# Performance work log

Hardware: AMD Instinct MI355X
Metric: run time of the kernel (lower is better)

## Reference

```python
import jax, jax.numpy as jnp
import numpy as np

B, N, S, VOCAB, D, NNZ = 16, 2048, 4096, 50257, 128, 1048576


def setup_inputs() -> dict:
    key = jax.random.key(0)
    k1, k2, k3, k4, k5, k6 = jax.random.split(key, 6)
    return {
        "subnode_ids": jax.random.randint(k1, (B, S), 0, VOCAB),
        "mask_batch": jax.random.randint(k2, (NNZ,), 0, B),
        "mask_node": jax.random.randint(k3, (NNZ,), 0, N),
        "mask_subnode": jax.random.randint(k4, (NNZ,), 0, S),
        "mask_values": jax.random.uniform(k5, (NNZ,), dtype=jnp.float32),
        "emb_table": jax.random.normal(k6, (VOCAB, D), dtype=jnp.float32),
    }


def reference(subnode_ids, mask_batch, mask_node, mask_subnode, mask_values, emb_table):
    # Gather token embeddings for every (batch, subnode) slot: [B, S, D] -> [B*S, D]
    subnode_emb = emb_table[subnode_ids].reshape(B * S, D)
    # Flattened COO indices (same as batch*max_nodes + node, batch*max_subnodes + subnode)
    row = mask_batch * N + mask_node      # destination node slot in [0, B*N)
    col = mask_batch * S + mask_subnode   # source subnode slot in [0, B*S)
    # Fused gather + weighted scatter-add (== sparse.mm of expanded_mask @ subnode_emb)
    contrib = subnode_emb[col] * mask_values[:, None]           # [NNZ, D]
    pooled = jax.ops.segment_sum(contrib, row, num_segments=B * N)  # [B*N, D]
    return pooled.reshape(B, N, D)
```

## Files before the change

### kernel.cpp

```cpp
#include <hip/hip_runtime.h>
#include <hip/hip_fp16.h>

#define Bq 16
#define Nq 2048
#define Sq 4096
#define Dq 128
#define VOCABq 50257
#define NNZq 1048576
#define ROWS (Bq * Nq)
#define NBIN 2048
#define RPB 16
#define BCAP 768
#define OVF_MAX 65536
#define BTPB 1024
#define BEPT 4

typedef unsigned long long u64;
typedef float vfloat4 __attribute__((ext_vector_type(4)));
typedef unsigned short vushort4 __attribute__((ext_vector_type(4)));
typedef unsigned short vushort8 __attribute__((ext_vector_type(8)));

__global__ __launch_bounds__(256) void cast_kernel(
    const float* __restrict__ emb, unsigned short* __restrict__ emb16)
{
    const int NQUAD = (VOCABq * Dq) / 4;
    int i = blockIdx.x * 256 + threadIdx.x;
    if (i >= NQUAD) return;
    vfloat4 f = reinterpret_cast<const vfloat4*>(emb)[i];
    vushort4 h;
    h.x = __half_as_ushort(__float2half_rn(f.x));
    h.y = __half_as_ushort(__float2half_rn(f.y));
    h.z = __half_as_ushort(__float2half_rn(f.z));
    h.w = __half_as_ushort(__float2half_rn(f.w));
    __builtin_nontemporal_store(h, reinterpret_cast<vushort4*>(emb16) + i);
}

__global__ __launch_bounds__(BTPB) void bin_kernel(
    const int* __restrict__ subnode_ids,
    const int* __restrict__ mb,
    const int* __restrict__ mn,
    const int* __restrict__ ms,
    const float* __restrict__ mv,
    int* __restrict__ binCnt,
    u64* __restrict__ binMem,
    int* __restrict__ ovfn,
    int* __restrict__ ovf)
{
    __shared__ int hist[NBIN];
    __shared__ int base[NBIN];
    int t = threadIdx.x;
    for (int g = t; g < NBIN; g += BTPB) hist[g] = 0;
    __syncthreads();

    int blockBase = blockIdx.x * (BTPB * BEPT);
    int g[BEPT], rank[BEPT];
    u64 pk[BEPT];
    #pragma unroll
    for (int k = 0; k < BEPT; k++) {
        int i   = blockBase + k * BTPB + t;
        int b   = mb[i];
        int row = b * Nq + mn[i];
        int tok = subnode_ids[b * Sq + ms[i]];
        float v = mv[i];
        g[k]  = row >> 4;
        pk[k] = ((u64)(unsigned)__float_as_int(v) << 32)
              | ((u64)(row & 15) << 16)
              | (unsigned)tok;
        rank[k] = atomicAdd(&hist[g[k]], 1);
    }
    __syncthreads();
    for (int gg = t; gg < NBIN; gg += BTPB) {
        int h = hist[gg];
        base[gg] = h ? atomicAdd(&binCnt[gg], h) : 0;
    }
    __syncthreads();
    #pragma unroll
    for (int k = 0; k < BEPT; k++) {
        int p = base[g[k]] + rank[k];
        if (p < BCAP) {
            binMem[(size_t)g[k] * BCAP + p] = pk[k];
        } else {
            int o = atomicAdd(ovfn, 1);
            if (o < OVF_MAX) ovf[o] = blockBase + k * BTPB + t;
        }
    }
}

__global__ __launch_bounds__(256) void pool_kernel(
    const unsigned short* __restrict__ emb16,
    const int* __restrict__ binCnt,
    const u64* __restrict__ binMem,
    float* __restrict__ out)
{
    __shared__ u64 ebuf[BCAP];
    __shared__ int hist[64];
    __shared__ int start[65];
    __shared__ int cursor[64];

    int t   = threadIdx.x;
    int bin = blockIdx.x;
    if (t < 64) hist[t] = 0;
    __syncthreads();

    int n = min(binCnt[bin], BCAP);
    const u64* bm = binMem + (size_t)bin * BCAP;

    u64 myPk[3];
    int myKey[3], myCnt = 0;
    for (int e = t; e < n; e += 256) {
        u64 pk  = bm[e];
        int tok = (int)(pk & 0xFFFF);
        int key = ((tok >> 14) << 4) | (int)((pk >> 16) & 15);
        myPk[myCnt] = pk; myKey[myCnt] = key; myCnt++;
        atomicAdd(&hist[key], 1);
    }
    __syncthreads();
    if (t < 64) {
        int v = hist[t];
        #pragma unroll
        for (int d = 1; d < 64; d <<= 1) {
            int w = __shfl_up(v, d, 64);
            if (t >= d) v += w;
        }
        start[t + 1] = v;
        if (t == 0) start[0] = 0;
    }
    __syncthreads();
    if (t < 64) cursor[t] = start[t];
    __syncthreads();
    for (int k = 0; k < myCnt; k++) {
        int p = atomicAdd(&cursor[myKey[k]], 1);
        ebuf[p] = myPk[k];
    }
    __syncthreads();

    int g    = t >> 4;
    int lane = t & 15;
    vfloat4 a0 = {0.f, 0.f, 0.f, 0.f};
    vfloat4 a1 = {0.f, 0.f, 0.f, 0.f};
    #pragma unroll
    for (int q = 0; q < 4; q++) {
        int s0 = start[q * 16 + g], s1 = start[q * 16 + g + 1];
        int k = s0;
        for (; k + 8 <= s1; k += 8) {
            int   tk[8];
            float vv[8];
            #pragma unroll
            for (int u = 0; u < 8; u++) {
                u64 pk = ebuf[k + u];
                tk[u] = (int)(pk & 0xFFFF);
                vv[u] = __int_as_float((int)(pk >> 32));
            }
            vushort8 e[8];
            #pragma unroll
            for (int u = 0; u < 8; u++)
                e[u] = reinterpret_cast<const vushort8*>(emb16 + (size_t)tk[u] * Dq)[lane];
            #pragma unroll
            for (int u = 0; u < 8; u++) {
                a0.x += __half2float(__ushort_as_half(e[u][0])) * vv[u];
                a0.y += __half2float(__ushort_as_half(e[u][1])) * vv[u];
                a0.z += __half2float(__ushort_as_half(e[u][2])) * vv[u];
                a0.w += __half2float(__ushort_as_half(e[u][3])) * vv[u];
                a1.x += __half2float(__ushort_as_half(e[u][4])) * vv[u];
                a1.y += __half2float(__ushort_as_half(e[u][5])) * vv[u];
                a1.z += __half2float(__ushort_as_half(e[u][6])) * vv[u];
                a1.w += __half2float(__ushort_as_half(e[u][7])) * vv[u];
            }
        }
        for (; k < s1; k++) {
            u64 pk = ebuf[k];
            int   tok = (int)(pk & 0xFFFF);
            float v   = __int_as_float((int)(pk >> 32));
            vushort8 e = reinterpret_cast<const vushort8*>(emb16 + (size_t)tok * Dq)[lane];
            a0.x += __half2float(__ushort_as_half(e[0])) * v;
            a0.y += __half2float(__ushort_as_half(e[1])) * v;
            a0.z += __half2float(__ushort_as_half(e[2])) * v;
            a0.w += __half2float(__ushort_as_half(e[3])) * v;
            a1.x += __half2float(__ushort_as_half(e[4])) * v;
            a1.y += __half2float(__ushort_as_half(e[5])) * v;
            a1.z += __half2float(__ushort_as_half(e[6])) * v;
            a1.w += __half2float(__ushort_as_half(e[7])) * v;
        }
    }
    float* orow = out + ((size_t)bin * RPB + g) * Dq + lane * 8;
    __builtin_nontemporal_store(a0, reinterpret_cast<vfloat4*>(orow));
    __builtin_nontemporal_store(a1, reinterpret_cast<vfloat4*>(orow) + 1);
}

__global__ __launch_bounds__(256) void overflow_kernel(
    const int* __restrict__ subnode_ids,
    const int* __restrict__ mb, const int* __restrict__ mn,
    const int* __restrict__ ms, const float* __restrict__ mv,
    const float* __restrict__ emb,
    const int* __restrict__ ovfn, const int* __restrict__ ovf,
    float* __restrict__ out)
{
    int nov = min(*ovfn, OVF_MAX);
    for (int e = blockIdx.x * 256 + threadIdx.x; e < nov; e += gridDim.x * 256) {
        int i = ovf[e];
        int b = mb[i];
        int row = b * Nq + mn[i];
        int tok = subnode_ids[b * Sq + ms[i]];
        float v = mv[i];
        const float* src = emb + (size_t)tok * Dq;
        float* dst = out + (size_t)row * Dq;
        for (int d = 0; d < Dq; d++) unsafeAtomicAdd(dst + d, src[d] * v);
    }
}

extern "C" void kernel_launch(void* const* d_in, const int* in_sizes, int n_in,
                              void* d_out, int out_size, void* d_ws, size_t ws_size,
                              hipStream_t stream) {
    const int*   subnode_ids  = (const int*)d_in[0];
    const int*   mask_batch   = (const int*)d_in[1];
    const int*   mask_node    = (const int*)d_in[2];
    const int*   mask_subnode = (const int*)d_in[3];
    const float* mask_values  = (const float*)d_in[4];
    const float* emb_table    = (const float*)d_in[5];
    float*       out          = (float*)d_out;

    unsigned short* emb16 = (unsigned short*)d_ws;
    u64* binMem = (u64*)(emb16 + (size_t)VOCABq * Dq + 64 );
    int* binCnt = (int*)(binMem + (size_t)NBIN * BCAP);
    int* ovfn   = binCnt + NBIN;
    int* ovf    = ovfn + 64;

    (void)hipMemsetAsync(binCnt, 0, (NBIN + 64) * sizeof(int), stream);

    const int NQUAD = (VOCABq * Dq) / 4;
    cast_kernel<<<(NQUAD + 255) / 256, 256, 0, stream>>>(emb_table, emb16);
    bin_kernel<<<NNZq / (BTPB * BEPT), BTPB, 0, stream>>>(
        subnode_ids, mask_batch, mask_node, mask_subnode, mask_values,
        binCnt, binMem, ovfn, ovf);
    pool_kernel<<<NBIN, 256, 0, stream>>>(emb16, binCnt, binMem, out);
    overflow_kernel<<<32, 256, 0, stream>>>(
        subnode_ids, mask_batch, mask_node, mask_subnode, mask_values,
        emb_table, ovfn, ovf, out);
}
```

Baseline: 137.7 us.

## Use coarser 64-row bins with 512-thread pool blocks handling two rows each

Bins now cover 64 output rows instead of 16, so there are 512 bins with a larger per-bin capacity. The pool kernel runs 512 threads per block, and each 16-lane group accumulates two rows. The in-block key sort grows from 64 to 256 keys and uses a shared-memory scan with barriers instead of a single-wavefront shuffle scan. The aim is to cut per-bin overheads and global bin-counter contention, at the cost of fewer, heavier blocks (possibly lower occupancy), a barrier-heavy scan, and more load imbalance per block.

After: 141.9 us. 1.03x slower.

```diff
diff --git a/kernel.cpp b/kernel.cpp
--- a/kernel.cpp
+++ b/kernel.cpp
@@ -8,12 +8,13 @@
 #define VOCABq 50257
 #define NNZq 1048576
 #define ROWS (Bq * Nq)
-#define NBIN 2048
-#define RPB 16
-#define BCAP 768
+#define NBIN 512
+#define RPB 64
+#define BCAP 2432
 #define OVF_MAX 65536
 #define BTPB 1024
-#define BEPT 4
+#define PTPB 512
+#define NKEY 256
 
 typedef unsigned long long u64;
 typedef float vfloat4 __attribute__((ext_vector_type(4)));
@@ -52,19 +53,19 @@
     for (int g = t; g < NBIN; g += BTPB) hist[g] = 0;
     __syncthreads();
 
-    int blockBase = blockIdx.x * (BTPB * BEPT);
-    int g[BEPT], rank[BEPT];
-    u64 pk[BEPT];
-    #pragma unroll
-    for (int k = 0; k < BEPT; k++) {
+    int blockBase = blockIdx.x * 4096;
+    int g[4], rank[4];
+    u64 pk[4];
+    #pragma unroll
+    for (int k = 0; k < 4; k++) {
         int i   = blockBase + k * BTPB + t;
         int b   = mb[i];
         int row = b * Nq + mn[i];
         int tok = subnode_ids[b * Sq + ms[i]];
         float v = mv[i];
-        g[k]  = row >> 4;
+        g[k]  = row >> 6;
         pk[k] = ((u64)(unsigned)__float_as_int(v) << 32)
-              | ((u64)(row & 15) << 16)
+              | ((u64)(row & 63) << 16)
               | (unsigned)tok;
         rank[k] = atomicAdd(&hist[g[k]], 1);
     }
@@ -75,7 +76,7 @@
     }
     __syncthreads();
     #pragma unroll
-    for (int k = 0; k < BEPT; k++) {
+    for (int k = 0; k < 4; k++) {
         int p = base[g[k]] + rank[k];
         if (p < BCAP) {
             binMem[(size_t)g[k] * BCAP + p] = pk[k];
@@ -86,105 +87,113 @@
     }
 }
 
-__global__ __launch_bounds__(256) void pool_kernel(
+__global__ __launch_bounds__(PTPB) void pool_kernel(
     const unsigned short* __restrict__ emb16,
     const int* __restrict__ binCnt,
     const u64* __restrict__ binMem,
     float* __restrict__ out)
 {
     __shared__ u64 ebuf[BCAP];
-    __shared__ int hist[64];
-    __shared__ int start[65];
-    __shared__ int cursor[64];
+    __shared__ int hist[NKEY];
+    __shared__ int start[NKEY + 1];
+    __shared__ int cursor[NKEY];
 
     int t   = threadIdx.x;
     int bin = blockIdx.x;
-    if (t < 64) hist[t] = 0;
+    if (t < NKEY) hist[t] = 0;
     __syncthreads();
 
     int n = min(binCnt[bin], BCAP);
     const u64* bm = binMem + (size_t)bin * BCAP;
 
-    u64 myPk[3];
-    int myKey[3], myCnt = 0;
-    for (int e = t; e < n; e += 256) {
+    u64 myPk[6];
+    int myKey[6], myCnt = 0;
+    for (int e = t; e < n && myCnt < 6; e += PTPB) {
         u64 pk  = bm[e];
         int tok = (int)(pk & 0xFFFF);
-        int key = ((tok >> 14) << 4) | (int)((pk >> 16) & 15);
+        int key = ((tok >> 14) << 6) | (int)((pk >> 16) & 63);
         myPk[myCnt] = pk; myKey[myCnt] = key; myCnt++;
         atomicAdd(&hist[key], 1);
     }
     __syncthreads();
-    if (t < 64) {
-        int v = hist[t];
-        #pragma unroll
-        for (int d = 1; d < 64; d <<= 1) {
-            int w = __shfl_up(v, d, 64);
-            if (t >= d) v += w;
-        }
-        start[t + 1] = v;
-        if (t == 0) start[0] = 0;
-    }
-    __syncthreads();
-    if (t < 64) cursor[t] = start[t];
+    for (int d = 1; d < NKEY; d <<= 1) {
+        int v = 0;
+        if (t < NKEY && t >= d) v = hist[t - d];
+        __syncthreads();
+        if (t < NKEY && t >= d) hist[t] += v;
+        __syncthreads();
+    }
+    if (t < NKEY) { start[t + 1] = hist[t]; cursor[t] = (t == 0) ? 0 : hist[t - 1]; }
+    if (t == 0) start[0] = 0;
     __syncthreads();
     for (int k = 0; k < myCnt; k++) {
         int p = atomicAdd(&cursor[myKey[k]], 1);
-        ebuf[p] = myPk[k];
+        if (p < BCAP) ebuf[p] = myPk[k];
     }
     __syncthreads();
 
     int g    = t >> 4;
     int lane = t & 15;
-    vfloat4 a0 = {0.f, 0.f, 0.f, 0.f};
-    vfloat4 a1 = {0.f, 0.f, 0.f, 0.f};
+    vfloat4 acc[2][2];
+    acc[0][0] = {0.f,0.f,0.f,0.f}; acc[0][1] = {0.f,0.f,0.f,0.f};
+    acc[1][0] = {0.f,0.f,0.f,0.f}; acc[1][1] = {0.f,0.f,0.f,0.f};
+
     #pragma unroll
     for (int q = 0; q < 4; q++) {
-        int s0 = start[q * 16 + g], s1 = start[q * 16 + g + 1];
-        int k = s0;
-        for (; k + 8 <= s1; k += 8) {
-            int   tk[8];
-            float vv[8];
-            #pragma unroll
-            for (int u = 0; u < 8; u++) {
-                u64 pk = ebuf[k + u];
-                tk[u] = (int)(pk & 0xFFFF);
-                vv[u] = __int_as_float((int)(pk >> 32));
+        #pragma unroll
+        for (int rr = 0; rr < 2; rr++) {
+            int r  = g * 2 + rr;
+            int s0 = start[q * 64 + r], s1 = start[q * 64 + r + 1];
+            vfloat4 a0 = acc[rr][0], a1 = acc[rr][1];
+            int k = s0;
+            for (; k + 8 <= s1; k += 8) {
+                int   tk[8];
+                float vv[8];
+                #pragma unroll
+                for (int u = 0; u < 8; u++) {
+                    u64 pk = ebuf[k + u];
+                    tk[u] = (int)(pk & 0xFFFF);
+                    vv[u] = __int_as_float((int)(pk >> 32));
+                }
+                vushort8 e[8];
+                #pragma unroll
+                for (int u = 0; u < 8; u++)
+                    e[u] = reinterpret_cast<const vushort8*>(emb16 + (size_t)tk[u] * Dq)[lane];
+                #pragma unroll
+                for (int u = 0; u < 8; u++) {
+                    a0.x += __half2float(__ushort_as_half(e[u][0])) * vv[u];
+                    a0.y += __half2float(__ushort_as_half(e[u][1])) * vv[u];
+                    a0.z += __half2float(__ushort_as_half(e[u][2])) * vv[u];
+                    a0.w += __half2float(__ushort_as_half(e[u][3])) * vv[u];
+                    a1.x += __half2float(__ushort_as_half(e[u][4])) * vv[u];
+                    a1.y += __half2float(__ushort_as_half(e[u][5])) * vv[u];
+                    a1.z += __half2float(__ushort_as_half(e[u][6])) * vv[u];
+                    a1.w += __half2float(__ushort_as_half(e[u][7])) * vv[u];
+                }
             }
-            vushort8 e[8];
-            #pragma unroll
-            for (int u = 0; u < 8; u++)
-                e[u] = reinterpret_cast<const vushort8*>(emb16 + (size_t)tk[u] * Dq)[lane];
-            #pragma unroll
-            for (int u = 0; u < 8; u++) {
-                a0.x += __half2float(__ushort_as_half(e[u][0])) * vv[u];
-                a0.y += __half2float(__ushort_as_half(e[u][1])) * vv[u];
-                a0.z += __half2float(__ushort_as_half(e[u][2])) * vv[u];
-                a0.w += __half2float(__ushort_as_half(e[u][3])) * vv[u];
-                a1.x += __half2float(__ushort_as_half(e[u][4])) * vv[u];
-                a1.y += __half2float(__ushort_as_half(e[u][5])) * vv[u];
-                a1.z += __half2float(__ushort_as_half(e[u][6])) * vv[u];
-                a1.w += __half2float(__ushort_as_half(e[u][7])) * vv[u];
+            for (; k < s1; k++) {
+                u64 pk = ebuf[k];
+                int   tok = (int)(pk & 0xFFFF);
+                float v   = __int_as_float((int)(pk >> 32));
+                vushort8 e = reinterpret_cast<const vushort8*>(emb16 + (size_t)tok * Dq)[lane];
+                a0.x += __half2float(__ushort_as_half(e[0])) * v;
+                a0.y += __half2float(__ushort_as_half(e[1])) * v;
+                a0.z += __half2float(__ushort_as_half(e[2])) * v;
+                a0.w += __half2float(__ushort_as_half(e[3])) * v;
+                a1.x += __half2float(__ushort_as_half(e[4])) * v;
+                a1.y += __half2float(__ushort_as_half(e[5])) * v;
+                a1.z += __half2float(__ushort_as_half(e[6])) * v;
+                a1.w += __half2float(__ushort_as_half(e[7])) * v;
             }
+            acc[rr][0] = a0; acc[rr][1] = a1;
         }
-        for (; k < s1; k++) {
-            u64 pk = ebuf[k];
-            int   tok = (int)(pk & 0xFFFF);
-            float v   = __int_as_float((int)(pk >> 32));
-            vushort8 e = reinterpret_cast<const vushort8*>(emb16 + (size_t)tok * Dq)[lane];
-            a0.x += __half2float(__ushort_as_half(e[0])) * v;
-            a0.y += __half2float(__ushort_as_half(e[1])) * v;
-            a0.z += __half2float(__ushort_as_half(e[2])) * v;
-            a0.w += __half2float(__ushort_as_half(e[3])) * v;
-            a1.x += __half2float(__ushort_as_half(e[4])) * v;
-            a1.y += __half2float(__ushort_as_half(e[5])) * v;
-            a1.z += __half2float(__ushort_as_half(e[6])) * v;
-            a1.w += __half2float(__ushort_as_half(e[7])) * v;
-        }
-    }
-    float* orow = out + ((size_t)bin * RPB + g) * Dq + lane * 8;
-    __builtin_nontemporal_store(a0, reinterpret_cast<vfloat4*>(orow));
-    __builtin_nontemporal_store(a1, reinterpret_cast<vfloat4*>(orow) + 1);
+    }
+    #pragma unroll
+    for (int rr = 0; rr < 2; rr++) {
+        float* orow = out + ((size_t)bin * RPB + g * 2 + rr) * Dq + lane * 8;
+        __builtin_nontemporal_store(acc[rr][0], reinterpret_cast<vfloat4*>(orow));
+        __builtin_nontemporal_store(acc[rr][1], reinterpret_cast<vfloat4*>(orow) + 1);
+    }
 }
 
 __global__ __launch_bounds__(256) void overflow_kernel(
@@ -229,10 +238,10 @@
 
     const int NQUAD = (VOCABq * Dq) / 4;
     cast_kernel<<<(NQUAD + 255) / 256, 256, 0, stream>>>(emb_table, emb16);
-    bin_kernel<<<NNZq / (BTPB * BEPT), BTPB, 0, stream>>>(
+    bin_kernel<<<NNZq / 4096, BTPB, 0, stream>>>(
         subnode_ids, mask_batch, mask_node, mask_subnode, mask_values,
         binCnt, binMem, ovfn, ovf);
-    pool_kernel<<<NBIN, 256, 0, stream>>>(emb16, binCnt, binMem, out);
+    pool_kernel<<<NBIN, PTPB, 0, stream>>>(emb16, binCnt, binMem, out);
     overflow_kernel<<<32, 256, 0, stream>>>(
         subnode_ids, mask_batch, mask_node, mask_subnode, mask_values,
         emb_table, ovfn, ovf, out);
```

## Coarsen COO bins to 64 rows and split pooling into four sub-blocks

Applied to the files above, without the earlier changes.

Nonzeros are now binned into 512 bins of 64 output rows instead of 2048 bins of 16 rows. This cuts the global bin-counter atomics per binning block and lengthens the contiguous runs each block writes into a bin. The pool kernel launches four blocks per bin. Each block scans the whole bin, keeps only the entries for its 16-row slice, and reads the bin from global memory twice instead of caching entries in registers. The trade-off is about four times the bin-read traffic during pooling. Entries beyond the 1024-slot shared buffer are silently dropped, though random inputs should stay well under that limit.

New measurement: 140.6 us. +2.1%, slower.

```diff
diff --git a/kernel.cpp b/kernel.cpp
--- a/kernel.cpp
+++ b/kernel.cpp
@@ -8,12 +8,12 @@
 #define VOCABq 50257
 #define NNZq 1048576
 #define ROWS (Bq * Nq)
-#define NBIN 2048
-#define RPB 16
-#define BCAP 768
+#define NBIN 512
+#define RPB 64
+#define BCAP 2432
 #define OVF_MAX 65536
 #define BTPB 1024
-#define BEPT 4
+#define EBUF 1024
 
 typedef unsigned long long u64;
 typedef float vfloat4 __attribute__((ext_vector_type(4)));
@@ -52,19 +52,19 @@
     for (int g = t; g < NBIN; g += BTPB) hist[g] = 0;
     __syncthreads();
 
-    int blockBase = blockIdx.x * (BTPB * BEPT);
-    int g[BEPT], rank[BEPT];
-    u64 pk[BEPT];
+    int blockBase = blockIdx.x * 4096;
+    int g[4], rank[4];
+    u64 pk[4];
     #pragma unroll
-    for (int k = 0; k < BEPT; k++) {
+    for (int k = 0; k < 4; k++) {
         int i   = blockBase + k * BTPB + t;
         int b   = mb[i];
         int row = b * Nq + mn[i];
         int tok = subnode_ids[b * Sq + ms[i]];
         float v = mv[i];
-        g[k]  = row >> 4;
+        g[k]  = row >> 6;
         pk[k] = ((u64)(unsigned)__float_as_int(v) << 32)
-              | ((u64)(row & 15) << 16)
+              | ((u64)(row & 63) << 16)
               | (unsigned)tok;
         rank[k] = atomicAdd(&hist[g[k]], 1);
     }
@@ -75,7 +75,7 @@
     }
     __syncthreads();
     #pragma unroll
-    for (int k = 0; k < BEPT; k++) {
+    for (int k = 0; k < 4; k++) {
         int p = base[g[k]] + rank[k];
         if (p < BCAP) {
             binMem[(size_t)g[k] * BCAP + p] = pk[k];
@@ -92,27 +92,27 @@
     const u64* __restrict__ binMem,
     float* __restrict__ out)
 {
-    __shared__ u64 ebuf[BCAP];
+    __shared__ u64 ebuf[EBUF];
     __shared__ int hist[64];
     __shared__ int start[65];
     __shared__ int cursor[64];
 
     int t   = threadIdx.x;
-    int bin = blockIdx.x;
+    int bin = blockIdx.x >> 2;
+    int sub = blockIdx.x & 3;
     if (t < 64) hist[t] = 0;
     __syncthreads();
 
     int n = min(binCnt[bin], BCAP);
     const u64* bm = binMem + (size_t)bin * BCAP;
 
-    u64 myPk[3];
-    int myKey[3], myCnt = 0;
     for (int e = t; e < n; e += 256) {
-        u64 pk  = bm[e];
-        int tok = (int)(pk & 0xFFFF);
-        int key = ((tok >> 14) << 4) | (int)((pk >> 16) & 15);
-        myPk[myCnt] = pk; myKey[myCnt] = key; myCnt++;
-        atomicAdd(&hist[key], 1);
+        u64 pk = bm[e];
+        int rl = (int)((pk >> 16) & 63);
+        if ((rl >> 4) == sub) {
+            int tok = (int)(pk & 0xFFFF);
+            atomicAdd(&hist[((tok >> 14) << 4) | (rl & 15)], 1);
+        }
     }
     __syncthreads();
     if (t < 64) {
@@ -128,9 +128,15 @@
     __syncthreads();
     if (t < 64) cursor[t] = start[t];
     __syncthreads();
-    for (int k = 0; k < myCnt; k++) {
-        int p = atomicAdd(&cursor[myKey[k]], 1);
-        ebuf[p] = myPk[k];
+    for (int e = t; e < n; e += 256) {
+        u64 pk = bm[e];
+        int rl = (int)((pk >> 16) & 63);
+        if ((rl >> 4) == sub) {
+            int tok = (int)(pk & 0xFFFF);
+            int key = ((tok >> 14) << 4) | (rl & 15);
+            int p = atomicAdd(&cursor[key], 1);
+            if (p < EBUF) ebuf[p] = pk;
+        }
     }
     __syncthreads();
 
@@ -182,7 +188,7 @@
             a1.w += __half2float(__ushort_as_half(e[7])) * v;
         }
     }
-    float* orow = out + ((size_t)bin * RPB + g) * Dq + lane * 8;
+    float* orow = out + ((size_t)bin * RPB + sub * 16 + g) * Dq + lane * 8;
     __builtin_nontemporal_store(a0, reinterpret_cast<vfloat4*>(orow));
     __builtin_nontemporal_store(a1, reinterpret_cast<vfloat4*>(orow) + 1);
 }
@@ -229,10 +235,10 @@
 
     const int NQUAD = (VOCABq * Dq) / 4;
     cast_kernel<<<(NQUAD + 255) / 256, 256, 0, stream>>>(emb_table, emb16);
-    bin_kernel<<<NNZq / (BTPB * BEPT), BTPB, 0, stream>>>(
+    bin_kernel<<<NNZq / 4096, BTPB, 0, stream>>>(
         subnode_ids, mask_batch, mask_node, mask_subnode, mask_values,
         binCnt, binMem, ovfn, ovf);
-    pool_kernel<<<NBIN, 256, 0, stream>>>(emb16, binCnt, binMem, out);
+    pool_kernel<<<NBIN * 4, 256, 0, stream>>>(emb16, binCnt, binMem, out);
     overflow_kernel<<<32, 256, 0, stream>>>(
         subnode_ids, mask_batch, mask_node, mask_subnode, mask_values,
         emb_table, ovfn, ovf, out);
```
